# Kernel optimization log

Measured on AMD Instinct MI355X. Metric: run time of the kernel, lower is better.

The kernel has to match this reference:

```python
import jax, jax.numpy as jnp
import numpy as np

D_MODEL = 256
NHEAD = 8
D_HEAD = D_MODEL // NHEAD
DIM_FF = 1024
B, L = 4, 16384
LN_EPS = 1e-5


def _layernorm(x, g, b):
    mu = jnp.mean(x, axis=-1, keepdims=True)
    var = jnp.mean((x - mu) ** 2, axis=-1, keepdims=True)
    return (x - mu) * jax.lax.rsqrt(var + LN_EPS) * g + b


def _phi(x):
    # elu(x) + 1
    return jnp.where(x > 0, x + 1.0, jnp.exp(x))


def setup_inputs() -> dict:
    key = jax.random.key(0)
    ks = jax.random.split(key, 16)
    s_in = 1.0 / np.sqrt(D_MODEL)
    s_ff = 1.0 / np.sqrt(DIM_FF)
    inp = {
        "x": jax.random.normal(ks[0], (B, L, D_MODEL), dtype=jnp.float32),
        "Wq": jax.random.normal(ks[1], (D_MODEL, D_MODEL), dtype=jnp.float32) * s_in,
        "bq": jnp.zeros((D_MODEL,), jnp.float32),
        "Wk": jax.random.normal(ks[2], (D_MODEL, D_MODEL), dtype=jnp.float32) * s_in,
        "bk": jnp.zeros((D_MODEL,), jnp.float32),
        "Wv": jax.random.normal(ks[3], (D_MODEL, D_MODEL), dtype=jnp.float32) * s_in,
        "bv": jnp.zeros((D_MODEL,), jnp.float32),
        "Wo": jax.random.normal(ks[4], (D_MODEL, D_MODEL), dtype=jnp.float32) * s_in,
        "bo": jnp.zeros((D_MODEL,), jnp.float32),
        "W1": jax.random.normal(ks[5], (D_MODEL, DIM_FF), dtype=jnp.float32) * s_in,
        "b1": jnp.zeros((DIM_FF,), jnp.float32),
        "W2": jax.random.normal(ks[6], (DIM_FF, D_MODEL), dtype=jnp.float32) * s_ff,
        "b2": jnp.zeros((D_MODEL,), jnp.float32),
        "ln1_g": jnp.ones((D_MODEL,), jnp.float32),
        "ln1_b": jnp.zeros((D_MODEL,), jnp.float32),
        "ln2_g": jnp.ones((D_MODEL,), jnp.float32),
        "ln2_b": jnp.zeros((D_MODEL,), jnp.float32),
    }
    return inp


def reference(x, Wq, bq, Wk, bk, Wv, bv, Wo, bo, W1, b1, W2, b2, ln1_g, ln1_b, ln2_g, ln2_b):
    Bq, Lq, _ = x.shape
    q = (x @ Wq + bq).reshape(Bq, Lq, NHEAD, D_HEAD)
    k = (x @ Wk + bk).reshape(Bq, Lq, NHEAD, D_HEAD)
    v = (x @ Wv + bv).reshape(Bq, Lq, NHEAD, D_HEAD)
    q_phi = _phi(q)
    k_phi = _phi(k)
    # kv: [B, H, d, e]
    kv = jnp.einsum("blhd,blhe->bhde", k_phi, v)
    k_sum = k_phi.sum(axis=1)  # [B, H, d]
    z = 1.0 / (jnp.einsum("blhd,bhd->blh", q_phi, k_sum) + 1e-6)
    out = jnp.einsum("blhd,bhde,blh->blhe", q_phi, kv, z)
    out = out.reshape(Bq, Lq, D_MODEL) @ Wo + bo
    x = _layernorm(x + out, ln1_g, ln1_b)
    ff = jax.nn.relu(x @ W1 + b1) @ W2 + b2
    x = _layernorm(x + ff, ln2_g, ln2_b)
    return x
```

## Files before the change

kernel.cpp:

```cpp
#include <hip/hip_runtime.h>
#include <hip/hip_bf16.h>
#include <math.h>

#define NTOK   65536
#define L_SEQ  16384

typedef __bf16 bf16_t;
typedef bf16_t bf16x8 __attribute__((ext_vector_type(8)));
typedef bf16_t bf16x4 __attribute__((ext_vector_type(4)));
typedef float  f32x4  __attribute__((ext_vector_type(4)));

__device__ inline float phi_f(float x) { return x > 0.f ? x + 1.f : __expf(x); }

__device__ inline float quad_sum(float v) {
    v += __shfl_xor(v, 1);
    v += __shfl_xor(v, 2);
    v += __shfl_xor(v, 4);
    v += __shfl_xor(v, 8);
    return v;
}

__device__ inline float ld_any(const void* p, size_t i, int f32) {
    return f32 ? ((const float*)p)[i] : (float)((const bf16_t*)p)[i];
}

__device__ inline void async_copy16(const bf16_t* g, bf16_t* l) {
    __builtin_amdgcn_global_load_lds(
        (const __attribute__((address_space(1))) unsigned int*)g,
        (__attribute__((address_space(3))) unsigned int*)l, 16, 0, 0);
}

__device__ inline void stage_swz(const bf16_t* __restrict__ g, bf16_t* lds,
                                 int tid, int nslot, int ulog2, int rowstride) {
    const int umask = (1 << ulog2) - 1;
    for (int s = tid; s < nslot; s += 256) {
        int n = s >> ulog2, j = s & umask;
        int u = j ^ (n & umask);
        async_copy16(g + (size_t)n * rowstride + u * 8, lds + (size_t)s * 8);
    }
}

__device__ inline bf16x8 rd_swz(const bf16_t* lds, int n, int u, int ulog2) {
    int j = u ^ (n & ((1 << ulog2) - 1));
    return *(const bf16x8*)&lds[(((size_t)n << ulog2) + j) * 8];
}

__device__ inline void stage_w2ff(const bf16_t* __restrict__ W2_t, int ch,
                                  bf16_t* lds, int tid) {
    for (int S = tid; S < 1024; S += 256) {
        int r = S >> 3, phys = S & 7;
        int u = phys ^ (r & 7);
        int n = ((u >> 2) << 7) + r;
        int ks = u & 3;
        async_copy16(W2_t + (size_t)n * 1024 + ch * 32 + ks * 8, lds + (size_t)S * 8);
    }
}

__device__ inline bf16x8 rd_w2ff(const bf16_t* lds, int n, int quad) {
    int r = n & 127;
    int u = ((n >> 7) << 2) + quad;
    int phys = u ^ (r & 7);
    return *(const bf16x8*)&lds[(size_t)(r * 8 + phys) * 8];
}

__device__ inline void ld_afrags(const bf16_t* __restrict__ tile, int row, int q8,
                                 bf16x8 a[8]) {
#pragma unroll
    for (int kk = 0; kk < 8; ++kk)
        a[kk] = *(const bf16x8*)&tile[(size_t)row * 256 + kk * 32 + q8];
}

__global__ __launch_bounds__(256) void k_detect(const void* __restrict__ xraw,
                                                int* __restrict__ flag) {
    __shared__ int bad;
    if (threadIdx.x == 0) bad = 0;
    __syncthreads();
    const bf16_t* xb = (const bf16_t*)xraw;
    int mybad = 0;
#pragma unroll
    for (int j = 0; j < 16; ++j) {
        float v = fabsf((float)xb[threadIdx.x + 256 * j]);
        if (!(v <= 1000.f)) mybad = 1;
    }
    if (mybad) atomicOr(&bad, 1);
    __syncthreads();
    if (threadIdx.x == 0) *flag = bad;
}

__global__ __launch_bounds__(256) void k_convert(const void* __restrict__ xraw,
                                                 const int* __restrict__ flag,
                                                 bf16_t* __restrict__ xbf) {
    const int f = *flag;
    size_t i = ((size_t)blockIdx.x * 256 + threadIdx.x) * 4;
    if (f) {
        f32x4 v = *(const f32x4*)((const float*)xraw + i);
        bf16x4 o;
#pragma unroll
        for (int j = 0; j < 4; ++j) o[j] = (bf16_t)v[j];
        *(bf16x4*)&xbf[i] = o;
    } else {
        *(bf16x4*)&xbf[i] = *(const bf16x4*)((const bf16_t*)xraw + i);
    }
}

__global__ __launch_bounds__(256) void k_prep(
    const void* __restrict__ Wq, const void* __restrict__ Wk,
    const void* __restrict__ Wv, const void* __restrict__ Wo,
    const void* __restrict__ W1, const void* __restrict__ W2,
    const void* __restrict__ bq, const void* __restrict__ bk,
    const void* __restrict__ bv, const void* __restrict__ bo,
    const void* __restrict__ b1, const void* __restrict__ b2,
    const void* __restrict__ g1, const void* __restrict__ be1,
    const void* __restrict__ g2, const void* __restrict__ be2,
    const int* __restrict__ flag,
    bf16_t* __restrict__ Wqkv_t, bf16_t* __restrict__ Wo_t,
    bf16_t* __restrict__ W1_t, bf16_t* __restrict__ W2_t,
    bf16_t* __restrict__ pbuf, float* __restrict__ kvbuf) {
    const int f = *flag;
    int idx = blockIdx.x * 256 + threadIdx.x;
    if (idx < 196608) {
        int n = idx >> 8, k = idx & 255;
        float v;
        if (n < 256)      v = ld_any(Wq, k * 256 + n, f);
        else if (n < 512) v = ld_any(Wk, k * 256 + (n - 256), f);
        else              v = ld_any(Wv, k * 256 + (n - 512), f);
        Wqkv_t[idx] = (bf16_t)v;
    } else if (idx < 262144) {
        int i = idx - 196608; int n = i >> 8, k = i & 255;
        Wo_t[i] = (bf16_t)ld_any(Wo, k * 256 + n, f);
    } else if (idx < 524288) {
        int i = idx - 262144; int n = i >> 8, k = i & 255;
        W1_t[i] = (bf16_t)ld_any(W1, k * 1024 + n, f);
    } else if (idx < 786432) {
        int i = idx - 524288; int n = i >> 10, k = i & 1023;
        W2_t[i] = (bf16_t)ld_any(W2, k * 256 + n, f);
    } else if (idx < 820224) {
        kvbuf[idx - 786432] = 0.f;
    } else if (idx < 823552) {
        int i = idx - 820224;
        float v;
        if (i < 256)        v = ld_any(bq, i, f);
        else if (i < 512)   v = ld_any(bk, i - 256, f);
        else if (i < 768)   v = ld_any(bv, i - 512, f);
        else if (i < 1024)  v = ld_any(bo, i - 768, f);
        else if (i < 2048)  v = ld_any(b1, i - 1024, f);
        else if (i < 2304)  v = ld_any(b2, i - 2048, f);
        else if (i < 2560)  v = ld_any(g1, i - 2304, f);
        else if (i < 2816)  v = ld_any(be1, i - 2560, f);
        else if (i < 3072)  v = ld_any(g2, i - 2816, f);
        else                v = ld_any(be2, i - 3072, f);
        pbuf[i] = (bf16_t)v;
    }
}

__global__ __launch_bounds__(256, 3) void k_qkv(
    const bf16_t* __restrict__ x, const bf16_t* __restrict__ Wqkv_t,
    const bf16_t* __restrict__ pbuf,
    bf16_t* __restrict__ q_phi, bf16_t* __restrict__ k_phi,
    bf16_t* __restrict__ v_out) {
    const int mt = blockIdx.x, nt = blockIdx.y;
    const int tid = threadIdx.x, wave = tid >> 6, lane = tid & 63;
    const int l15 = lane & 15, quad = lane >> 4, q8 = quad * 8;
    __shared__ __align__(16) bf16_t bs[128 * 256];
    const int m0 = mt * 128;
    bf16x8 a[2][8];
    ld_afrags(x + (size_t)m0 * 256,        wave * 16 + l15, q8, a[0]);
    ld_afrags(x + (size_t)(m0 + 64) * 256, wave * 16 + l15, q8, a[1]);
    stage_swz(Wqkv_t + (size_t)nt * 128 * 256, bs, tid, 4096, 5, 256);
    __syncthreads();
    f32x4 acc[2][8] = {};
#pragma unroll
    for (int kk = 0; kk < 8; ++kk) {
#pragma unroll
        for (int s = 0; s < 8; ++s) {
            bf16x8 b = rd_swz(bs, s * 16 + l15, kk * 4 + quad, 5);
            acc[0][s] = __builtin_amdgcn_mfma_f32_16x16x32_bf16(a[0][kk], b, acc[0][s], 0, 0, 0);
            acc[1][s] = __builtin_amdgcn_mfma_f32_16x16x32_bf16(a[1][kk], b, acc[1][s], 0, 0, 0);
        }
    }
#pragma unroll
    for (int s = 0; s < 8; ++s) {
        int ng = nt * 128 + s * 16 + l15;
        bf16_t* dst = ng < 256 ? q_phi : (ng < 512 ? k_phi : v_out);
        int nl = ng & 255;
        float bias = (float)pbuf[(ng < 256 ? 0 : (ng < 512 ? 256 : 512)) + nl];
#pragma unroll
        for (int mm = 0; mm < 2; ++mm) {
#pragma unroll
            for (int r = 0; r < 4; ++r) {
                int m = m0 + mm * 64 + wave * 16 + quad * 4 + r;
                float val = acc[mm][s][r] + bias;
                if (ng < 512) val = phi_f(val);
                dst[(size_t)m * 256 + nl] = (bf16_t)val;
            }
        }
    }
}

__global__ __launch_bounds__(256) void k_kvsum(
    const bf16_t* __restrict__ k_phi, const bf16_t* __restrict__ v_in,
    float* __restrict__ kvbuf) {
    const int bid = blockIdx.x;
    const int bh = bid >> 6, ck = bid & 63;
    const int b = bh >> 3, h = bh & 7;
    const int tid = threadIdx.x;
    __shared__ float ks[32][33], vs[32][33];
    const size_t base = ((size_t)b * L_SEQ + ck * 256) * 256 + h * 32;
    const int row = tid >> 3, c4 = (tid & 7) * 4;
    const int d = row, e4 = c4;
    float acc[4] = {}, ksacc = 0.f;
    for (int it = 0; it < 8; ++it) {
        bf16x4 kk4 = *(const bf16x4*)&k_phi[base + (size_t)(it * 32 + row) * 256 + c4];
        bf16x4 vv4 = *(const bf16x4*)&v_in[base + (size_t)(it * 32 + row) * 256 + c4];
#pragma unroll
        for (int j = 0; j < 4; ++j) { ks[row][c4 + j] = (float)kk4[j]; vs[row][c4 + j] = (float)vv4[j]; }
        __syncthreads();
#pragma unroll
        for (int ii = 0; ii < 32; ++ii) {
            float kd = ks[ii][d];
            ksacc += kd;
#pragma unroll
            for (int j = 0; j < 4; ++j) acc[j] += kd * vs[ii][e4 + j];
        }
        __syncthreads();
    }
    float* kvdst = kvbuf + (size_t)bh * 1056;
#pragma unroll
    for (int j = 0; j < 4; ++j) atomicAdd(&kvdst[(e4 + j) * 32 + d], acc[j]);
    if ((tid & 7) == 0) atomicAdd(&kvdst[1024 + d], ksacc);
}

__global__ __launch_bounds__(256) void k_kvprep(const float* __restrict__ kvbuf,
                                                bf16_t* __restrict__ kvbf) {
    int idx = blockIdx.x * 256 + threadIdx.x;
    int bh = idx >> 8, r4 = (idx & 255) * 4;
    f32x4 v = *(const f32x4*)&kvbuf[(size_t)bh * 1056 + r4];
    bf16x4 o;
#pragma unroll
    for (int j = 0; j < 4; ++j) o[j] = (bf16_t)v[j];
    *(bf16x4*)&kvbf[(size_t)bh * 1024 + r4] = o;
}

__global__ __launch_bounds__(256, 2) void k_attn_wo_ln1(
    const bf16_t* __restrict__ q_phi, const bf16_t* __restrict__ kvbf,
    const float* __restrict__ kvbuf, const bf16_t* __restrict__ Wo_t,
    const bf16_t* __restrict__ pbuf, const void* __restrict__ xraw,
    const int* __restrict__ flag, bf16_t* __restrict__ x1) {
    const int f = *flag;
    const int mt = blockIdx.x;
    const int tid = threadIdx.x, wave = tid >> 6, lane = tid & 63;
    const int l15 = lane & 15, quad = lane >> 4, q8 = quad * 8;
    __shared__ __align__(16) bf16_t sm0[8192];
    __shared__ __align__(16) bf16_t sm1[16896];
    const int m0 = mt * 128;
    const int b = m0 >> 14;
    stage_swz(Wo_t, sm0, tid, 1024, 5, 256);
    bf16_t* hs = sm1 + wave * (16 * 264);
    const bf16_t* kvb = kvbf + (size_t)b * 8192;
    const float*  ksb = kvbuf + (size_t)b * 8448;
    bf16x8 a2[2][8];
#pragma unroll
    for (int mm = 0; mm < 2; ++mm) {
        bf16x8 a[8];
        ld_afrags(q_phi + (size_t)(m0 + mm * 64) * 256, wave * 16 + l15, q8, a);
#pragma unroll
        for (int h = 0; h < 8; ++h) {
            f32x4 ks0 = *(const f32x4*)&ksb[h * 1056 + 1024 + q8];
            f32x4 ks1 = *(const f32x4*)&ksb[h * 1056 + 1024 + q8 + 4];
            float den = 0.f;
#pragma unroll
            for (int j = 0; j < 4; ++j) den += (float)a[h][j] * ks0[j];
#pragma unroll
            for (int j = 0; j < 4; ++j) den += (float)a[h][4 + j] * ks1[j];
            den += __shfl_xor(den, 16);
            den += __shfl_xor(den, 32);
            float z = 1.f / (den + 1e-6f);
            float zr[4];
#pragma unroll
            for (int r = 0; r < 4; ++r) zr[r] = __shfl(z, quad * 4 + r, 16);
            bf16x8 b0 = *(const bf16x8*)&kvb[h * 1024 + l15 * 32 + q8];
            bf16x8 b1 = *(const bf16x8*)&kvb[h * 1024 + (16 + l15) * 32 + q8];
            f32x4 at0 = {}, at1 = {};
            at0 = __builtin_amdgcn_mfma_f32_16x16x32_bf16(a[h], b0, at0, 0, 0, 0);
            at1 = __builtin_amdgcn_mfma_f32_16x16x32_bf16(a[h], b1, at1, 0, 0, 0);
#pragma unroll
            for (int r = 0; r < 4; ++r) {
                hs[(quad * 4 + r) * 264 + h * 32 + l15]      = (bf16_t)(at0[r] * zr[r]);
                hs[(quad * 4 + r) * 264 + h * 32 + 16 + l15] = (bf16_t)(at1[r] * zr[r]);
            }
        }
#pragma unroll
        for (int kk = 0; kk < 8; ++kk)
            a2[mm][kk] = *(const bf16x8*)&hs[l15 * 264 + kk * 32 + q8];
    }
    __syncthreads();
    f32x4 acc[2][16] = {};
    for (int nc = 0; nc < 8; ++nc) {
        if (nc < 7) stage_swz(Wo_t + (size_t)(nc + 1) * 32 * 256,
                              (nc & 1) ? sm0 : sm1, tid, 1024, 5, 256);
        const bf16_t* buf = (nc & 1) ? sm1 : sm0;
#pragma unroll
        for (int kk = 0; kk < 8; ++kk) {
#pragma unroll
            for (int s = 0; s < 2; ++s) {
                bf16x8 bb = rd_swz(buf, s * 16 + l15, kk * 4 + quad, 5);
                acc[0][nc * 2 + s] = __builtin_amdgcn_mfma_f32_16x16x32_bf16(a2[0][kk], bb, acc[0][nc * 2 + s], 0, 0, 0);
                acc[1][nc * 2 + s] = __builtin_amdgcn_mfma_f32_16x16x32_bf16(a2[1][kk], bb, acc[1][nc * 2 + s], 0, 0, 0);
            }
        }
        __syncthreads();
    }
#pragma unroll
    for (int mm = 0; mm < 2; ++mm) {
        float s1[4] = {}, s2[4] = {};
#pragma unroll
        for (int s = 0; s < 16; ++s) {
            int n = s * 16 + l15;
            float bias = (float)pbuf[768 + n];
#pragma unroll
            for (int r = 0; r < 4; ++r) {
                int m = m0 + mm * 64 + wave * 16 + quad * 4 + r;
                float val = acc[mm][s][r] + bias + ld_any(xraw, (size_t)m * 256 + n, f);
                acc[mm][s][r] = val;
                s1[r] += val; s2[r] += val * val;
            }
        }
#pragma unroll
        for (int r = 0; r < 4; ++r) {
            float ts = quad_sum(s1[r]), ts2 = quad_sum(s2[r]);
            float mu = ts * (1.f / 256.f);
            float rs = rsqrtf(ts2 * (1.f / 256.f) - mu * mu + 1e-5f);
            s1[r] = mu; s2[r] = rs;
        }
#pragma unroll
        for (int s = 0; s < 16; ++s) {
            int n = s * 16 + l15;
            float gn = (float)pbuf[2304 + n], bn = (float)pbuf[2560 + n];
#pragma unroll
            for (int r = 0; r < 4; ++r) {
                int m = m0 + mm * 64 + wave * 16 + quad * 4 + r;
                x1[(size_t)m * 256 + n] = (bf16_t)((acc[mm][s][r] - s1[r]) * s2[r] * gn + bn);
            }
        }
    }
}

__global__ __launch_bounds__(256, 2) void k_ff_ln2(
    const bf16_t* __restrict__ x1, const bf16_t* __restrict__ W1_t,
    const bf16_t* __restrict__ W2_t, const bf16_t* __restrict__ pbuf,
    const int* __restrict__ flag, void* __restrict__ out) {
    const int f32o = *flag;
    const int mt = blockIdx.x;
    const int tid = threadIdx.x, wave = tid >> 6, lane = tid & 63;
    const int l15 = lane & 15, quad = lane >> 4, q8 = quad * 8;
    __shared__ __align__(16) bf16_t w1s[2][8192];
    __shared__ __align__(16) bf16_t w2s[2][8192];
    __shared__ __align__(16) bf16_t hs[4][2][16][40];
    const int m0 = mt * 128 + wave * 32;
    bf16x8 a[2][8];
    ld_afrags(x1 + (size_t)m0 * 256, l15,      q8, a[0]);
    ld_afrags(x1 + (size_t)m0 * 256, 16 + l15, q8, a[1]);
    stage_swz(W1_t, w1s[0], tid, 1024, 5, 256);
    stage_w2ff(W2_t, 0, w2s[0], tid);
    __syncthreads();
    f32x4 acc[2][16] = {};
    for (int ch = 0; ch < 32; ++ch) {
        const int cur = ch & 1;
        if (ch < 31) {
            stage_swz(W1_t + (size_t)(ch + 1) * 32 * 256, w1s[cur ^ 1], tid, 1024, 5, 256);
            stage_w2ff(W2_t, ch + 1, w2s[cur ^ 1], tid);
        }
        f32x4 h0[2] = {}, h1[2] = {};
#pragma unroll
        for (int kk = 0; kk < 8; ++kk) {
#pragma unroll
            for (int s = 0; s < 2; ++s) {
                bf16x8 b = rd_swz(w1s[cur], s * 16 + l15, kk * 4 + quad, 5);
                h0[s] = __builtin_amdgcn_mfma_f32_16x16x32_bf16(a[0][kk], b, h0[s], 0, 0, 0);
                h1[s] = __builtin_amdgcn_mfma_f32_16x16x32_bf16(a[1][kk], b, h1[s], 0, 0, 0);
            }
        }
#pragma unroll
        for (int s = 0; s < 2; ++s) {
            float bias = (float)pbuf[1024 + ch * 32 + s * 16 + l15];
#pragma unroll
            for (int r = 0; r < 4; ++r) {
                float v0 = h0[s][r] + bias;
                float v1 = h1[s][r] + bias;
                hs[wave][0][quad * 4 + r][s * 16 + l15] = (bf16_t)(v0 > 0.f ? v0 : 0.f);
                hs[wave][1][quad * 4 + r][s * 16 + l15] = (bf16_t)(v1 > 0.f ? v1 : 0.f);
            }
        }
        bf16x8 a2_0 = *(const bf16x8*)&hs[wave][0][l15][q8];
        bf16x8 a2_1 = *(const bf16x8*)&hs[wave][1][l15][q8];
#pragma unroll
        for (int s = 0; s < 16; ++s) {
            bf16x8 b0 = rd_w2ff(w2s[cur], s * 16 + l15, quad);
            acc[0][s] = __builtin_amdgcn_mfma_f32_16x16x32_bf16(a2_0, b0, acc[0][s], 0, 0, 0);
            acc[1][s] = __builtin_amdgcn_mfma_f32_16x16x32_bf16(a2_1, b0, acc[1][s], 0, 0, 0);
        }
        __syncthreads();
    }
#pragma unroll
    for (int mm = 0; mm < 2; ++mm) {
        float s1[4] = {}, s2[4] = {};
#pragma unroll
        for (int s = 0; s < 16; ++s) {
            int n = s * 16 + l15;
            float bias = (float)pbuf[2048 + n];
#pragma unroll
            for (int r = 0; r < 4; ++r) {
                int m = m0 + mm * 16 + quad * 4 + r;
                float val = acc[mm][s][r] + bias + (float)x1[(size_t)m * 256 + n];
                acc[mm][s][r] = val;
                s1[r] += val; s2[r] += val * val;
            }
        }
#pragma unroll
        for (int r = 0; r < 4; ++r) {
            float ts = quad_sum(s1[r]), ts2 = quad_sum(s2[r]);
            float mu = ts * (1.f / 256.f);
            float rs = rsqrtf(ts2 * (1.f / 256.f) - mu * mu + 1e-5f);
            s1[r] = mu; s2[r] = rs;
        }
#pragma unroll
        for (int s = 0; s < 16; ++s) {
            int n = s * 16 + l15;
            float gn = (float)pbuf[2816 + n], bn = (float)pbuf[3072 + n];
#pragma unroll
            for (int r = 0; r < 4; ++r) {
                int m = m0 + mm * 16 + quad * 4 + r;
                float val = (acc[mm][s][r] - s1[r]) * s2[r] * gn + bn;
                if (f32o) ((float*)out)[(size_t)m * 256 + n] = val;
                else      ((bf16_t*)out)[(size_t)m * 256 + n] = (bf16_t)val;
            }
        }
    }
}

extern "C" void kernel_launch(void* const* d_in, const int* in_sizes, int n_in,
                              void* d_out, int out_size, void* d_ws, size_t ws_size,
                              hipStream_t stream) {
    char* ws = (char*)d_ws;
    int*    flag   = (int*)ws;
    bf16_t* xbf    = (bf16_t*)(ws + 256);
    bf16_t* Wqkv_t = (bf16_t*)(ws + 33554688);
    bf16_t* Wo_t   = (bf16_t*)(ws + 33947904);
    bf16_t* W1_t   = (bf16_t*)(ws + 34078976);
    bf16_t* W2_t   = (bf16_t*)(ws + 34603264);
    bf16_t* pbuf   = (bf16_t*)(ws + 35127552);
    float*  kvbuf  = (float*)(ws + 35134208);
    bf16_t* bufQ   = (bf16_t*)(ws + 35269376);
    bf16_t* bufK   = bufQ + (size_t)NTOK * 256;
    bf16_t* bufV   = bufK + (size_t)NTOK * 256;
    bf16_t* kvbf   = bufV;
    bf16_t* bufX1  = bufQ;

    k_detect<<<1, 256, 0, stream>>>(d_in[0], flag);
    k_convert<<<16384, 256, 0, stream>>>(d_in[0], flag, xbf);
    k_prep<<<3217, 256, 0, stream>>>(d_in[1], d_in[3], d_in[5], d_in[7],
                                     d_in[9], d_in[11],
                                     d_in[2], d_in[4], d_in[6], d_in[8],
                                     d_in[10], d_in[12],
                                     d_in[13], d_in[14], d_in[15], d_in[16],
                                     flag, Wqkv_t, Wo_t, W1_t, W2_t, pbuf, kvbuf);
    k_qkv<<<dim3(512, 6), 256, 0, stream>>>(xbf, Wqkv_t, pbuf, bufQ, bufK, bufV);
    k_kvsum<<<2048, 256, 0, stream>>>(bufK, bufV, kvbuf);
    k_kvprep<<<32, 256, 0, stream>>>(kvbuf, kvbf);
    k_attn_wo_ln1<<<512, 256, 0, stream>>>(bufQ, kvbf, kvbuf, Wo_t, pbuf,
                                           d_in[0], flag, bufX1);
    k_ff_ln2<<<512, 256, 0, stream>>>(bufX1, W1_t, W2_t, pbuf, flag, d_out);
}
```

Before: 404.8 us.

## Fuse K/V projection with KV reduction to avoid materializing K and V

The K and V projections move out of the QKV GEMM into a new kernel that computes per-head K_phi and V tiles into swizzled LDS and immediately reduces them into kv and k_sum with MFMA and atomics. This removes the global write and reread of the full K and V activations (two 32 MB bf16 buffers) and the separate kvsum kernel. The trade-off is more atomics per tile into kvbuf, serialized per-head staging with extra barriers, and K/V rounded to bf16 before the outer product.

```diff
diff --git a/kernel.cpp b/kernel.cpp
--- a/kernel.cpp
+++ b/kernel.cpp
@@ -61,6 +61,15 @@
     int u = ((n >> 7) << 2) + quad;
     int phys = u ^ (r & 7);
     return *(const bf16x8*)&lds[(size_t)(r * 8 + phys) * 8];
+}
+
+__device__ inline void hs_put(bf16_t* hs, int r, int c, bf16_t v) {
+    int phys = (c >> 3) ^ (r & 15);
+    hs[r * 128 + phys * 8 + (c & 7)] = v;
+}
+__device__ inline bf16x8 hs_get8(const bf16_t* hs, int r, int u) {
+    int phys = u ^ (r & 15);
+    return *(const bf16x8*)&hs[r * 128 + phys * 8];
 }
 
 __device__ inline void ld_afrags(const bf16_t* __restrict__ tile, int row, int q8,
@@ -155,9 +164,7 @@
 
 __global__ __launch_bounds__(256, 3) void k_qkv(
     const bf16_t* __restrict__ x, const bf16_t* __restrict__ Wqkv_t,
-    const bf16_t* __restrict__ pbuf,
-    bf16_t* __restrict__ q_phi, bf16_t* __restrict__ k_phi,
-    bf16_t* __restrict__ v_out) {
+    const bf16_t* __restrict__ pbuf, bf16_t* __restrict__ q_phi) {
     const int mt = blockIdx.x, nt = blockIdx.y;
     const int tid = threadIdx.x, wave = tid >> 6, lane = tid & 63;
     const int l15 = lane & 15, quad = lane >> 4, q8 = quad * 8;
@@ -181,53 +188,113 @@
 #pragma unroll
     for (int s = 0; s < 8; ++s) {
         int ng = nt * 128 + s * 16 + l15;
-        bf16_t* dst = ng < 256 ? q_phi : (ng < 512 ? k_phi : v_out);
-        int nl = ng & 255;
-        float bias = (float)pbuf[(ng < 256 ? 0 : (ng < 512 ? 256 : 512)) + nl];
+        float bias = (float)pbuf[ng];
 #pragma unroll
         for (int mm = 0; mm < 2; ++mm) {
 #pragma unroll
             for (int r = 0; r < 4; ++r) {
                 int m = m0 + mm * 64 + wave * 16 + quad * 4 + r;
-                float val = acc[mm][s][r] + bias;
-                if (ng < 512) val = phi_f(val);
-                dst[(size_t)m * 256 + nl] = (bf16_t)val;
-            }
-        }
-    }
-}
-
-__global__ __launch_bounds__(256) void k_kvsum(
-    const bf16_t* __restrict__ k_phi, const bf16_t* __restrict__ v_in,
-    float* __restrict__ kvbuf) {
-    const int bid = blockIdx.x;
-    const int bh = bid >> 6, ck = bid & 63;
-    const int b = bh >> 3, h = bh & 7;
-    const int tid = threadIdx.x;
-    __shared__ float ks[32][33], vs[32][33];
-    const size_t base = ((size_t)b * L_SEQ + ck * 256) * 256 + h * 32;
-    const int row = tid >> 3, c4 = (tid & 7) * 4;
-    const int d = row, e4 = c4;
-    float acc[4] = {}, ksacc = 0.f;
-    for (int it = 0; it < 8; ++it) {
-        bf16x4 kk4 = *(const bf16x4*)&k_phi[base + (size_t)(it * 32 + row) * 256 + c4];
-        bf16x4 vv4 = *(const bf16x4*)&v_in[base + (size_t)(it * 32 + row) * 256 + c4];
-#pragma unroll
-        for (int j = 0; j < 4; ++j) { ks[row][c4 + j] = (float)kk4[j]; vs[row][c4 + j] = (float)vv4[j]; }
+                q_phi[(size_t)m * 256 + ng] = (bf16_t)phi_f(acc[mm][s][r] + bias);
+            }
+        }
+    }
+}
+
+__global__ __launch_bounds__(256, 4) void k_kv(
+    const bf16_t* __restrict__ x, const bf16_t* __restrict__ Wqkv_t,
+    const bf16_t* __restrict__ pbuf, float* __restrict__ kvbuf) {
+    const int mt = blockIdx.x, hg = blockIdx.y;
+    const int tid = threadIdx.x, wave = tid >> 6, lane = tid & 63;
+    const int l15 = lane & 15, quad = lane >> 4, q8 = quad * 8;
+    __shared__ __align__(16) bf16_t stg[8192];
+    __shared__ __align__(16) bf16_t hsK[4096];
+    __shared__ __align__(16) bf16_t hsV[4096];
+    const int m0 = mt * 128;
+    const int b = m0 >> 14;
+    bf16x8 a[2][8];
+    ld_afrags(x + (size_t)m0 * 256,        wave * 16 + l15, q8, a[0]);
+    ld_afrags(x + (size_t)(m0 + 64) * 256, wave * 16 + l15, q8, a[1]);
+    const int td = wave >> 1, te = wave & 1;
+    for (int h4 = 0; h4 < 4; ++h4) {
+        const int head = hg * 4 + h4;
+        const size_t kvbase = (size_t)(b * 8 + head) * 1056;
+        stage_swz(Wqkv_t + (size_t)(256 + head * 32) * 256, stg, tid, 1024, 5, 256);
         __syncthreads();
-#pragma unroll
-        for (int ii = 0; ii < 32; ++ii) {
-            float kd = ks[ii][d];
-            ksacc += kd;
-#pragma unroll
-            for (int j = 0; j < 4; ++j) acc[j] += kd * vs[ii][e4 + j];
+        {
+            f32x4 acck[2][2] = {};
+#pragma unroll
+            for (int kk = 0; kk < 8; ++kk) {
+#pragma unroll
+                for (int s = 0; s < 2; ++s) {
+                    bf16x8 bb = rd_swz(stg, s * 16 + l15, kk * 4 + quad, 5);
+                    acck[0][s] = __builtin_amdgcn_mfma_f32_16x16x32_bf16(a[0][kk], bb, acck[0][s], 0, 0, 0);
+                    acck[1][s] = __builtin_amdgcn_mfma_f32_16x16x32_bf16(a[1][kk], bb, acck[1][s], 0, 0, 0);
+                }
+            }
+#pragma unroll
+            for (int s = 0; s < 2; ++s) {
+                float bias = (float)pbuf[256 + head * 32 + s * 16 + l15];
+                float kst = 0.f;
+#pragma unroll
+                for (int mm = 0; mm < 2; ++mm) {
+#pragma unroll
+                    for (int r = 0; r < 4; ++r) {
+                        float v = phi_f(acck[mm][s][r] + bias);
+                        kst += v;
+                        int c = mm * 64 + wave * 16 + quad * 4 + r;
+                        hs_put(hsK, s * 16 + l15, c, (bf16_t)v);
+                    }
+                }
+                kst += __shfl_xor(kst, 16);
+                kst += __shfl_xor(kst, 32);
+                if (quad == 0)
+                    atomicAdd(&kvbuf[kvbase + 1024 + s * 16 + l15], kst);
+            }
         }
         __syncthreads();
-    }
-    float* kvdst = kvbuf + (size_t)bh * 1056;
-#pragma unroll
-    for (int j = 0; j < 4; ++j) atomicAdd(&kvdst[(e4 + j) * 32 + d], acc[j]);
-    if ((tid & 7) == 0) atomicAdd(&kvdst[1024 + d], ksacc);
+        stage_swz(Wqkv_t + (size_t)(512 + head * 32) * 256, stg, tid, 1024, 5, 256);
+        __syncthreads();
+        {
+            f32x4 accv[2][2] = {};
+#pragma unroll
+            for (int kk = 0; kk < 8; ++kk) {
+#pragma unroll
+                for (int s = 0; s < 2; ++s) {
+                    bf16x8 bb = rd_swz(stg, s * 16 + l15, kk * 4 + quad, 5);
+                    accv[0][s] = __builtin_amdgcn_mfma_f32_16x16x32_bf16(a[0][kk], bb, accv[0][s], 0, 0, 0);
+                    accv[1][s] = __builtin_amdgcn_mfma_f32_16x16x32_bf16(a[1][kk], bb, accv[1][s], 0, 0, 0);
+                }
+            }
+#pragma unroll
+            for (int s = 0; s < 2; ++s) {
+                float bias = (float)pbuf[512 + head * 32 + s * 16 + l15];
+#pragma unroll
+                for (int mm = 0; mm < 2; ++mm) {
+#pragma unroll
+                    for (int r = 0; r < 4; ++r) {
+                        int c = mm * 64 + wave * 16 + quad * 4 + r;
+                        hs_put(hsV, s * 16 + l15, c, (bf16_t)(accv[mm][s][r] + bias));
+                    }
+                }
+            }
+        }
+        __syncthreads();
+        {
+            f32x4 kvacc = {};
+#pragma unroll
+            for (int kk = 0; kk < 4; ++kk) {
+                bf16x8 ak = hs_get8(hsK, td * 16 + l15, kk * 4 + quad);
+                bf16x8 bv = hs_get8(hsV, te * 16 + l15, kk * 4 + quad);
+                kvacc = __builtin_amdgcn_mfma_f32_16x16x32_bf16(ak, bv, kvacc, 0, 0, 0);
+            }
+#pragma unroll
+            for (int r = 0; r < 4; ++r) {
+                int d = td * 16 + quad * 4 + r;
+                int e = te * 16 + l15;
+                atomicAdd(&kvbuf[kvbase + e * 32 + d], kvacc[r]);
+            }
+        }
+    }
 }
 
 __global__ __launch_bounds__(256) void k_kvprep(const float* __restrict__ kvbuf,
@@ -451,9 +518,7 @@
     bf16_t* pbuf   = (bf16_t*)(ws + 35127552);
     float*  kvbuf  = (float*)(ws + 35134208);
     bf16_t* bufQ   = (bf16_t*)(ws + 35269376);
-    bf16_t* bufK   = bufQ + (size_t)NTOK * 256;
-    bf16_t* bufV   = bufK + (size_t)NTOK * 256;
-    bf16_t* kvbf   = bufV;
+    bf16_t* kvbf   = bufQ + (size_t)NTOK * 256;
     bf16_t* bufX1  = bufQ;
 
     k_detect<<<1, 256, 0, stream>>>(d_in[0], flag);
@@ -464,8 +529,8 @@
                                      d_in[10], d_in[12],
                                      d_in[13], d_in[14], d_in[15], d_in[16],
                                      flag, Wqkv_t, Wo_t, W1_t, W2_t, pbuf, kvbuf);
-    k_qkv<<<dim3(512, 6), 256, 0, stream>>>(xbf, Wqkv_t, pbuf, bufQ, bufK, bufV);
-    k_kvsum<<<2048, 256, 0, stream>>>(bufK, bufV, kvbuf);
+    k_qkv<<<dim3(512, 2), 256, 0, stream>>>(xbf, Wqkv_t, pbuf, bufQ);
+    k_kv<<<dim3(512, 2), 256, 0, stream>>>(xbf, Wqkv_t, pbuf, kvbuf);
     k_kvprep<<<32, 256, 0, stream>>>(kvbuf, kvbf);
     k_attn_wo_ln1<<<512, 256, 0, stream>>>(bufQ, kvbf, kvbuf, Wo_t, pbuf,
                                            d_in[0], flag, bufX1);
```

After: 440.2 us. 8.8% more time.
